# Kernel tuning notes

Hardware: AMD Instinct MI355X
Metric: run time of the kernel (lower is better)

Reference implementation:

```python
import jax, jax.numpy as jnp
import numpy as np

B, QL, KL, D, H = 2, 2048, 2048, 1024, 16
E = D // H  # head dim


def setup_inputs() -> dict:
    key = jax.random.key(0)
    ks = jax.random.split(key, 12)
    query_features = jax.random.normal(ks[0], (B, QL, D), dtype=jnp.float32)
    key_features = jax.random.normal(ks[1], (B, KL, D), dtype=jnp.float32)
    # causal additive mask [QL, KL]: -inf above the diagonal, 0 elsewhere
    dependency_mask = jnp.where(
        jnp.arange(KL)[None, :] > jnp.arange(QL)[:, None], -jnp.inf, 0.0
    ).astype(jnp.float32)
    # key padding: random valid lengths in [KL//2, KL]; True = padded position
    lengths = jax.random.randint(ks[2], (B,), KL // 2, KL + 1)
    key_padding_mask = jnp.arange(KL)[None, :] >= lengths[:, None]
    s = 0.02
    Wq = jax.random.normal(ks[3], (D, D), jnp.float32) * s
    bq = jax.random.normal(ks[4], (D,), jnp.float32) * s
    Wk = jax.random.normal(ks[5], (D, D), jnp.float32) * s
    bk = jax.random.normal(ks[6], (D,), jnp.float32) * s
    Wv = jax.random.normal(ks[7], (D, D), jnp.float32) * s
    bv = jax.random.normal(ks[8], (D,), jnp.float32) * s
    Wo = jax.random.normal(ks[9], (D, D), jnp.float32) * s
    bo = jax.random.normal(ks[10], (D,), jnp.float32) * s
    return dict(query_features=query_features, key_features=key_features,
                dependency_mask=dependency_mask, key_padding_mask=key_padding_mask,
                Wq=Wq, bq=bq, Wk=Wk, bk=bk, Wv=Wv, bv=bv, Wo=Wo, bo=bo)


def reference(query_features, key_features, dependency_mask, key_padding_mask,
              Wq, bq, Wk, bk, Wv, bv, Wo, bo):
    b, kl, d = key_features.shape
    ql = query_features.shape[1]
    q = query_features @ Wq.T + bq          # [B, QL, D]
    k = key_features @ Wk.T + bk            # [B, KL, D]
    v = key_features @ Wv.T + bv            # [B, KL, D]
    qh = q.reshape(b, ql, H, E)
    kh = k.reshape(b, kl, H, E)
    vh = v.reshape(b, kl, H, E)
    # NOTE: original scales by sqrt(d_model), not sqrt(head_dim)
    scores = jnp.einsum('bqhe,bkhe->bhqk', qh, kh) / jnp.sqrt(jnp.float32(d))
    scores = jnp.where(key_padding_mask[:, None, None, :], -jnp.inf, scores)
    scores = scores + dependency_mask  # broadcast [QL,KL] over [B,H,QL,KL]
    probs = jax.nn.softmax(scores, axis=-1)  # dropout is identity in eval mode
    agg = jnp.einsum('bhqk,bkhe->bqhe', probs, vh).reshape(b, ql, d)
    return agg @ Wo.T + bo
```

## Files before the change

### kernel.cpp

```cpp
#include <hip/hip_runtime.h>
#include <hip/hip_bf16.h>


typedef __bf16 bf16x8 __attribute__((ext_vector_type(8)));
typedef float f32x4 __attribute__((ext_vector_type(4)));
typedef unsigned int u32x4 __attribute__((ext_vector_type(4)));
typedef unsigned short u16;
typedef unsigned int u32;

#define GLOBAL_AS __attribute__((address_space(1)))
#define LDS_AS __attribute__((address_space(3)))

static __device__ __forceinline__ u16 f2bf(float f) {
    __hip_bfloat16 h = __float2bfloat16(f);
    return __builtin_bit_cast(u16, h);
}
static __device__ __forceinline__ u32 pack2bf(float a, float b) {
    return (u32)f2bf(a) | ((u32)f2bf(b) << 16);
}
static __device__ __forceinline__ float exp2_hw(float x) {
    return __builtin_amdgcn_exp2f(x);
}

__global__ void cvt_all(const float* __restrict__ xq_f, const float* __restrict__ xk_f,
                        const float* __restrict__ wq_f, const float* __restrict__ wk_f,
                        const float* __restrict__ wv_f, const float* __restrict__ wo_f,
                        u16* __restrict__ xq, u16* __restrict__ xk,
                        u16* __restrict__ wq, u16* __restrict__ wk,
                        u16* __restrict__ wv, u16* __restrict__ wo,
                        const int* __restrict__ kpm, int* __restrict__ lens) {
    int blk = blockIdx.x;
    if (blk >= 12288) {
        const int b = blk - 12288, tid = threadIdx.x;
        int cnt = 0;
        #pragma unroll
        for (int i = 0; i < 8; ++i) cnt += (kpm[b * 2048 + i * 256 + tid] == 0) ? 1 : 0;
        #pragma unroll
        for (int off = 32; off; off >>= 1) cnt += __shfl_down(cnt, off);
        __shared__ int wsum[4];
        if ((tid & 63) == 0) wsum[tid >> 6] = cnt;
        __syncthreads();
        if (tid == 0) lens[b] = wsum[0] + wsum[1] + wsum[2] + wsum[3];
        return;
    }
    const float* s; u16* d; int i;
    if (blk < 4096)      { s = xq_f; d = xq; i = blk * 256 + threadIdx.x; }
    else if (blk < 8192) { s = xk_f; d = xk; i = (blk - 4096) * 256 + threadIdx.x; }
    else {
        int wsel = (blk - 8192) >> 10;
        i = ((blk - 8192) & 1023) * 256 + threadIdx.x;
        if (wsel == 0)      { s = wq_f; d = wq; }
        else if (wsel == 1) { s = wk_f; d = wk; }
        else if (wsel == 2) { s = wv_f; d = wv; }
        else                { s = wo_f; d = wo; }
    }
    float4 v = reinterpret_cast<const float4*>(s)[i];
    ushort4 o;
    o.x = f2bf(v.x); o.y = f2bf(v.y); o.z = f2bf(v.z); o.w = f2bf(v.w);
    reinterpret_cast<ushort4*>(d)[i] = o;
}

template<int OUT_F32, int BM, int BN>
__device__ __forceinline__
void gemm_body(const u16* __restrict__ A, const u16* __restrict__ Bw,
               const float* __restrict__ bias, void* __restrict__ Cout,
               int N, int K, float scale, int bx, int by) {
    constexpr int MREP = BM / 32, NREP = BN / 32;
    constexpr int ACH = BM / 8, TCH = ACH + BN / 8;
    constexpr int CPW = TCH / 4;
    __shared__ __attribute__((aligned(16))) u16 aS[BM * 64];
    __shared__ __attribute__((aligned(16))) u16 bS[BN * 64];
    const int tid = threadIdx.x, wave = tid >> 6, lane = tid & 63;
    const int m0 = by * BM, n0 = bx * BN;
    const int wr = wave >> 1, wc = wave & 1;
    const int fr = lane & 15, fq = lane >> 4;
    const int swz_col = (((lane & 7) ^ (lane >> 3)) * 8);
    const int rsw = (fr & 7) << 3;

    f32x4 acc[MREP][NREP] = {};

    for (int k0 = 0; k0 < K; k0 += 64) {
        #pragma unroll
        for (int i = 0; i < CPW; ++i) {
            int chunk = wave * CPW + i;
            const u16* gsrc; u16* ldst;
            if (chunk < ACH) {
                int row = chunk * 8 + (lane >> 3);
                gsrc = A + (size_t)(m0 + row) * K + k0 + swz_col;
                ldst = aS + chunk * 512;
            } else {
                int row = (chunk - ACH) * 8 + (lane >> 3);
                gsrc = Bw + (size_t)(n0 + row) * K + k0 + swz_col;
                ldst = bS + (chunk - ACH) * 512;
            }
            __builtin_amdgcn_global_load_lds((GLOBAL_AS void*)gsrc,
                                             (LDS_AS void*)ldst, 16, 0, 0);
        }
        __syncthreads();
        bf16x8 af[MREP][2], bfr[NREP][2];
        #pragma unroll
        for (int m = 0; m < MREP; ++m)
            #pragma unroll
            for (int h = 0; h < 2; ++h)
                af[m][h] = *reinterpret_cast<const bf16x8*>(
                    &aS[(wr * (BM / 2) + m * 16 + fr) * 64 + ((h * 32 + fq * 8) ^ rsw)]);
        #pragma unroll
        for (int n = 0; n < NREP; ++n)
            #pragma unroll
            for (int h = 0; h < 2; ++h)
                bfr[n][h] = *reinterpret_cast<const bf16x8*>(
                    &bS[(wc * (BN / 2) + n * 16 + fr) * 64 + ((h * 32 + fq * 8) ^ rsw)]);
        __builtin_amdgcn_s_setprio(1);
        #pragma unroll
        for (int m = 0; m < MREP; ++m)
            #pragma unroll
            for (int n = 0; n < NREP; ++n) {
                acc[m][n] = __builtin_amdgcn_mfma_f32_16x16x32_bf16(af[m][0], bfr[n][0], acc[m][n], 0, 0, 0);
                acc[m][n] = __builtin_amdgcn_mfma_f32_16x16x32_bf16(af[m][1], bfr[n][1], acc[m][n], 0, 0, 0);
            }
        __builtin_amdgcn_s_setprio(0);
        __syncthreads();
    }

    #pragma unroll
    for (int n = 0; n < NREP; ++n) {
        int col = n0 + wc * (BN / 2) + n * 16 + fr;
        float bv = bias[col];
        #pragma unroll
        for (int m = 0; m < MREP; ++m) {
            #pragma unroll
            for (int j = 0; j < 4; ++j) {
                int row = m0 + wr * (BM / 2) + m * 16 + fq * 4 + j;
                float v = (acc[m][n][j] + bv) * scale;
                if (OUT_F32)
                    reinterpret_cast<float*>(Cout)[(size_t)row * N + col] = v;
                else
                    reinterpret_cast<u16*>(Cout)[(size_t)row * N + col] = f2bf(v);
            }
        }
    }
}

__global__ __launch_bounds__(256, 3)
void gemm_qkv(const u16* __restrict__ xq, const u16* __restrict__ xk,
              const u16* __restrict__ wq, const u16* __restrict__ wk,
              const u16* __restrict__ wv,
              const float* __restrict__ bq, const float* __restrict__ bk,
              const float* __restrict__ bv,
              u16* __restrict__ qb, u16* __restrict__ kb, u16* __restrict__ vb) {
    const int id = blockIdx.x;
    const int g = id & 7, s = id >> 3;
    const int z = s >> 5;
    const int xl = (s >> 3) & 3, byl = s & 7;
    const int bx = (g & 1) * 4 + xl;
    const int by = (g >> 1) * 8 + byl;
    const u16* A = (z == 0) ? xq : xk;
    const u16* W = (z == 0) ? wq : (z == 1) ? wk : wv;
    const float* bias = (z == 0) ? bq : (z == 1) ? bk : bv;
    u16* C = (z == 0) ? qb : (z == 1) ? kb : vb;
    const float scale = (z == 0) ? 0.0450842200f : 1.0f;
    gemm_body<0, 128, 128>(A, W, bias, C, 1024, 1024, scale, bx, by);
}

__global__ __launch_bounds__(256, 2)
void gemm_out(const u16* __restrict__ A, const u16* __restrict__ Bw,
              const float* __restrict__ bias, float* __restrict__ Cout) {
    const int id = blockIdx.x;
    const int g = id & 7, s = id >> 3;
    const int xl = s & 3, byl = s >> 2;
    const int bx = (g & 1) * 4 + xl;
    const int by = (g >> 1) * 16 + byl;
    gemm_body<1, 64, 128>(A, Bw, bias, Cout, 1024, 1024, 1.0f, bx, by);
}

__global__ __launch_bounds__(256, 4)
void attn_fwd(const u16* __restrict__ Qb, const u16* __restrict__ Kb,
              const u16* __restrict__ Vb, const int* __restrict__ lens,
              u16* __restrict__ Ob) {
    __shared__ __attribute__((aligned(16))) u16 Ks[2][64 * 64];
    __shared__ __attribute__((aligned(16))) u16 Vts[2][64 * 64];
    const int tid = threadIdx.x, wave = tid >> 6, lane = tid & 63;
    const int id = blockIdx.x;
    const int bh = (id & 7) * 4 + ((id >> 3) & 3);
    const int k5 = id >> 5;
    const int g = k5 >> 3, x8 = k5 & 7;
    const int qt = (g == 0) ? x8 : (g == 1) ? 31 - x8 : (g == 2) ? 16 + x8 : 15 - x8;
    const int b = bh >> 4, h = bh & 15;
    const int q0 = qt * 64;
    const int fr = lane & 15, fq = lane >> 4;
    const int qrow = q0 + wave * 16;
    const int len = lens[b];
    const int nt = min(qt + 1, (len + 63) >> 6);

    const size_t qoff = (size_t)(b * 2048 + qrow + fr) * 1024 + h * 64 + fq * 8;
    bf16x8 qa0 = *reinterpret_cast<const bf16x8*>(Qb + qoff);
    bf16x8 qa1 = *reinterpret_cast<const bf16x8*>(Qb + qoff + 32);

    bf16x8 ones;
    #pragma unroll
    for (int i = 0; i < 8; ++i) ones[i] = __builtin_bit_cast(__bf16, (u16)0x3F80);

    f32x4 o_acc[4] = {};
    f32x4 lacc = {};

    const int e8 = tid >> 5;
    const int c2 = tid & 31;
    const int kp = 2 * c2;
    const int vhalf = kp >> 5, r5 = kp & 31;
    const int fqv = r5 >> 3, nv = (r5 >> 2) & 1, jv = r5 & 3;
    const int k_src = vhalf * 32 + nv * 16 + fqv * 4 + jv;
    const int kswz_col = (((lane & 7) ^ (lane >> 3)) * 8);

    auto issue_K = [&](int kt, int buf) {
        #pragma unroll
        for (int i = 0; i < 2; ++i) {
            int chunk = wave * 2 + i;
            int krow = chunk * 8 + (lane >> 3);
            const u16* gk = Kb + (size_t)(b * 2048 + kt * 64 + krow) * 1024 + h * 64 + kswz_col;
            __builtin_amdgcn_global_load_lds((GLOBAL_AS void*)gk,
                                             (LDS_AS void*)(&Ks[buf][chunk * 512]), 16, 0, 0);
        }
    };
    auto load_V = [&](int kt, ushort4* r) {
        const u16* b1 = Vb + (size_t)(b * 2048 + kt * 64 + k_src) * 1024 + h * 64 + e8 * 8;
        r[0] = reinterpret_cast<const ushort4*>(b1)[0];
        r[1] = reinterpret_cast<const ushort4*>(b1 + 4)[0];
        r[2] = reinterpret_cast<const ushort4*>(b1 + 1024)[0];
        r[3] = reinterpret_cast<const ushort4*>(b1 + 1024 + 4)[0];
    };
    auto write_V = [&](const ushort4* r, int buf) {
        u32* vbase = reinterpret_cast<u32*>(&Vts[buf][0]);
        const u16* lo16 = reinterpret_cast<const u16*>(&r[0]);
        const u16* hi16 = reinterpret_cast<const u16*>(&r[2]);
        #pragma unroll
        for (int i = 0; i < 8; ++i) {
            u32 w = (u32)lo16[i] | ((u32)hi16[i] << 16);
            vbase[(e8 * 8 + i) * 32 + (c2 ^ (i << 2))] = w;
        }
    };

    {
        ushort4 vr[4];
        issue_K(0, 0);
        load_V(0, vr);
        write_V(vr, 0);
    }
    __syncthreads();

    for (int kt = 0; kt < nt; ++kt) {
        const int k0 = kt * 64;
        const int cur = kt & 1, nxt = cur ^ 1;
        const bool has_next = (kt + 1 < nt);

        ushort4 vr[4];
        if (has_next) {
            issue_K(kt + 1, nxt);
            load_V(kt + 1, vr);
        }

        f32x4 s[4] = {};
        __builtin_amdgcn_s_setprio(1);
        #pragma unroll
        for (int n = 0; n < 4; ++n) {
            int kr = n * 16 + fr;
            int sw = (fr & 7) << 3;
            bf16x8 kb0 = *reinterpret_cast<const bf16x8*>(&Ks[cur][kr * 64 + ((fq * 8) ^ sw)]);
            bf16x8 kb1 = *reinterpret_cast<const bf16x8*>(&Ks[cur][kr * 64 + ((32 + fq * 8) ^ sw)]);
            s[n] = __builtin_amdgcn_mfma_f32_16x16x32_bf16(kb0, qa0, s[n], 0, 0, 0);
            s[n] = __builtin_amdgcn_mfma_f32_16x16x32_bf16(kb1, qa1, s[n], 0, 0, 0);
        }
        __builtin_amdgcn_s_setprio(0);

        const bool fullt = (k0 + 63 <= qrow) && (k0 + 64 <= len);
        if (!fullt) {
            const int qg = qrow + fr;
            #pragma unroll
            for (int n = 0; n < 4; ++n)
                #pragma unroll
                for (int j = 0; j < 4; ++j) {
                    int kg = k0 + n * 16 + fq * 4 + j;
                    s[n][j] = (kg <= qg && kg < len) ? s[n][j] : -1e30f;
                }
        }
        #pragma unroll
        for (int n = 0; n < 4; ++n)
            #pragma unroll
            for (int j = 0; j < 4; ++j)
                s[n][j] = exp2_hw(s[n][j]);

        u32x4 w0, w1;
        w0[0] = pack2bf(s[0][0], s[0][1]); w0[1] = pack2bf(s[0][2], s[0][3]);
        w0[2] = pack2bf(s[1][0], s[1][1]); w0[3] = pack2bf(s[1][2], s[1][3]);
        w1[0] = pack2bf(s[2][0], s[2][1]); w1[1] = pack2bf(s[2][2], s[2][3]);
        w1[2] = pack2bf(s[3][0], s[3][1]); w1[3] = pack2bf(s[3][2], s[3][3]);
        bf16x8 pa0 = __builtin_bit_cast(bf16x8, w0);
        bf16x8 pa1 = __builtin_bit_cast(bf16x8, w1);

        if (has_next) write_V(vr, nxt);

        __builtin_amdgcn_s_setprio(1);
        lacc = __builtin_amdgcn_mfma_f32_16x16x32_bf16(pa0, ones, lacc, 0, 0, 0);
        #pragma unroll
        for (int n = 0; n < 4; ++n) {
            int vr2 = n * 16 + fr;
            bf16x8 vb2 = *reinterpret_cast<const bf16x8*>(
                &Vts[cur][vr2 * 64 + ((fq * 8) ^ ((fr & 7) << 3))]);
            o_acc[n] = __builtin_amdgcn_mfma_f32_16x16x32_bf16(pa0, vb2, o_acc[n], 0, 0, 0);
        }
        lacc = __builtin_amdgcn_mfma_f32_16x16x32_bf16(pa1, ones, lacc, 0, 0, 0);
        #pragma unroll
        for (int n = 0; n < 4; ++n) {
            int vr2 = n * 16 + fr;
            bf16x8 vb2 = *reinterpret_cast<const bf16x8*>(
                &Vts[cur][vr2 * 64 + ((32 + fq * 8) ^ ((fr & 7) << 3))]);
            o_acc[n] = __builtin_amdgcn_mfma_f32_16x16x32_bf16(pa1, vb2, o_acc[n], 0, 0, 0);
        }
        __builtin_amdgcn_s_setprio(0);

        __syncthreads();
    }

    #pragma unroll
    for (int j = 0; j < 4; ++j) {
        float inv = 1.f / lacc[j];
        int row = qrow + fq * 4 + j;
        #pragma unroll
        for (int n = 0; n < 4; ++n) {
            int col = h * 64 + n * 16 + fr;
            Ob[(size_t)(b * 2048 + row) * 1024 + col] = f2bf(o_acc[n][j] * inv);
        }
    }
}

extern "C" void kernel_launch(void* const* d_in, const int* in_sizes, int n_in,
                              void* d_out, int out_size, void* d_ws, size_t ws_size,
                              hipStream_t stream) {
    const float* xq_f = (const float*)d_in[0];
    const float* xk_f = (const float*)d_in[1];
    const int* kpm = (const int*)d_in[3];
    const float* Wq = (const float*)d_in[4];
    const float* bq = (const float*)d_in[5];
    const float* Wk = (const float*)d_in[6];
    const float* bk = (const float*)d_in[7];
    const float* Wv = (const float*)d_in[8];
    const float* bv = (const float*)d_in[9];
    const float* Wo = (const float*)d_in[10];
    const float* bo = (const float*)d_in[11];

    u16* ws = (u16*)d_ws;
    u16* xq = ws;
    u16* xk = xq + 4194304;
    u16* wq = xk + 4194304;
    u16* wk = wq + 1048576;
    u16* wv = wk + 1048576;
    u16* wo = wv + 1048576;
    u16* qb = wo + 1048576;
    u16* kb2 = qb + 4194304;
    u16* vb2 = kb2 + 4194304;
    u16* ag = vb2 + 4194304;
    int* lens = (int*)(ag + 4194304);

    cvt_all<<<12290, 256, 0, stream>>>(xq_f, xk_f, Wq, Wk, Wv, Wo,
                                       xq, xk, wq, wk, wv, wo, kpm, lens);

    gemm_qkv<<<768, 256, 0, stream>>>(xq, xk, wq, wk, wv,
                                      bq, bk, bv, qb, kb2, vb2);

    attn_fwd<<<1024, 256, 0, stream>>>(qb, kb2, vb2, lens, ag);

    gemm_out<<<512, 256, 0, stream>>>(ag, wo, bo, (float*)d_out);
}
```

Before: 100.6 us.

## Split attention tile across waves by key halves with LDS reduction

Each wave now handles 32 query rows against one 32-key half of each 64-key tile, instead of 16 query rows against all 64 keys. Every K and V fragment read from LDS is then reused for two query groups, which halves per-wave LDS fragment traffic. The price is a final cross-wave reduction of the partial O and row sums through LDS, with extra barriers, and more accumulator registers per wave.

```diff
diff --git a/kernel.cpp b/kernel.cpp
--- a/kernel.cpp
+++ b/kernel.cpp
@@ -186,22 +186,27 @@
     const int g = k5 >> 3, x8 = k5 & 7;
     const int qt = (g == 0) ? x8 : (g == 1) ? 31 - x8 : (g == 2) ? 16 + x8 : 15 - x8;
     const int b = bh >> 4, h = bh & 15;
-    const int q0 = qt * 64;
     const int fr = lane & 15, fq = lane >> 4;
-    const int qrow = q0 + wave * 16;
+    const int t = wave >> 1;
+    const int u = wave & 1;
+    const int qbase = qt * 64 + u * 32;
     const int len = lens[b];
     const int nt = min(qt + 1, (len + 63) >> 6);
 
-    const size_t qoff = (size_t)(b * 2048 + qrow + fr) * 1024 + h * 64 + fq * 8;
-    bf16x8 qa0 = *reinterpret_cast<const bf16x8*>(Qb + qoff);
-    bf16x8 qa1 = *reinterpret_cast<const bf16x8*>(Qb + qoff + 32);
+    bf16x8 qa[2][2];
+    #pragma unroll
+    for (int gq = 0; gq < 2; ++gq) {
+        const size_t qoff = (size_t)(b * 2048 + qbase + gq * 16 + fr) * 1024 + h * 64 + fq * 8;
+        qa[gq][0] = *reinterpret_cast<const bf16x8*>(Qb + qoff);
+        qa[gq][1] = *reinterpret_cast<const bf16x8*>(Qb + qoff + 32);
+    }
 
     bf16x8 ones;
     #pragma unroll
     for (int i = 0; i < 8; ++i) ones[i] = __builtin_bit_cast(__bf16, (u16)0x3F80);
 
-    f32x4 o_acc[4] = {};
-    f32x4 lacc = {};
+    f32x4 o_acc[2][4] = {};
+    f32x4 lacc[2] = {};
 
     const int e8 = tid >> 5;
     const int c2 = tid & 31;
@@ -249,6 +254,7 @@
 
     for (int kt = 0; kt < nt; ++kt) {
         const int k0 = kt * 64;
+        const int kbase = k0 + t * 32;
         const int cur = kt & 1, nxt = cur ^ 1;
         const bool has_next = (kt + 1 < nt);
 
@@ -258,77 +264,107 @@
             load_V(kt + 1, vr);
         }
 
-        f32x4 s[4] = {};
+        f32x4 s[2][2] = {};
         __builtin_amdgcn_s_setprio(1);
         #pragma unroll
-        for (int n = 0; n < 4; ++n) {
-            int kr = n * 16 + fr;
+        for (int kq2 = 0; kq2 < 2; ++kq2) {
+            int kr = t * 32 + kq2 * 16 + fr;
             int sw = (fr & 7) << 3;
             bf16x8 kb0 = *reinterpret_cast<const bf16x8*>(&Ks[cur][kr * 64 + ((fq * 8) ^ sw)]);
             bf16x8 kb1 = *reinterpret_cast<const bf16x8*>(&Ks[cur][kr * 64 + ((32 + fq * 8) ^ sw)]);
-            s[n] = __builtin_amdgcn_mfma_f32_16x16x32_bf16(kb0, qa0, s[n], 0, 0, 0);
-            s[n] = __builtin_amdgcn_mfma_f32_16x16x32_bf16(kb1, qa1, s[n], 0, 0, 0);
+            #pragma unroll
+            for (int gq = 0; gq < 2; ++gq) {
+                s[kq2][gq] = __builtin_amdgcn_mfma_f32_16x16x32_bf16(kb0, qa[gq][0], s[kq2][gq], 0, 0, 0);
+                s[kq2][gq] = __builtin_amdgcn_mfma_f32_16x16x32_bf16(kb1, qa[gq][1], s[kq2][gq], 0, 0, 0);
+            }
         }
         __builtin_amdgcn_s_setprio(0);
 
-        const bool fullt = (k0 + 63 <= qrow) && (k0 + 64 <= len);
+        const bool fullt = (kbase + 31 <= qbase) && (kbase + 32 <= len);
         if (!fullt) {
-            const int qg = qrow + fr;
-            #pragma unroll
-            for (int n = 0; n < 4; ++n)
+            #pragma unroll
+            for (int kq2 = 0; kq2 < 2; ++kq2)
                 #pragma unroll
-                for (int j = 0; j < 4; ++j) {
-                    int kg = k0 + n * 16 + fq * 4 + j;
-                    s[n][j] = (kg <= qg && kg < len) ? s[n][j] : -1e30f;
+                for (int gq = 0; gq < 2; ++gq) {
+                    int qg = qbase + gq * 16 + fr;
+                    #pragma unroll
+                    for (int j = 0; j < 4; ++j) {
+                        int kg = kbase + kq2 * 16 + fq * 4 + j;
+                        s[kq2][gq][j] = (kg <= qg && kg < len) ? s[kq2][gq][j] : -1e30f;
+                    }
                 }
         }
         #pragma unroll
-        for (int n = 0; n < 4; ++n)
-            #pragma unroll
-            for (int j = 0; j < 4; ++j)
-                s[n][j] = exp2_hw(s[n][j]);
-
-        u32x4 w0, w1;
-        w0[0] = pack2bf(s[0][0], s[0][1]); w0[1] = pack2bf(s[0][2], s[0][3]);
-        w0[2] = pack2bf(s[1][0], s[1][1]); w0[3] = pack2bf(s[1][2], s[1][3]);
-        w1[0] = pack2bf(s[2][0], s[2][1]); w1[1] = pack2bf(s[2][2], s[2][3]);
-        w1[2] = pack2bf(s[3][0], s[3][1]); w1[3] = pack2bf(s[3][2], s[3][3]);
-        bf16x8 pa0 = __builtin_bit_cast(bf16x8, w0);
-        bf16x8 pa1 = __builtin_bit_cast(bf16x8, w1);
+        for (int kq2 = 0; kq2 < 2; ++kq2)
+            #pragma unroll
+            for (int gq = 0; gq < 2; ++gq)
+                #pragma unroll
+                for (int j = 0; j < 4; ++j)
+                    s[kq2][gq][j] = exp2_hw(s[kq2][gq][j]);
+
+        bf16x8 pa[2];
+        #pragma unroll
+        for (int gq = 0; gq < 2; ++gq) {
+            u32x4 w;
+            w[0] = pack2bf(s[0][gq][0], s[0][gq][1]);
+            w[1] = pack2bf(s[0][gq][2], s[0][gq][3]);
+            w[2] = pack2bf(s[1][gq][0], s[1][gq][1]);
+            w[3] = pack2bf(s[1][gq][2], s[1][gq][3]);
+            pa[gq] = __builtin_bit_cast(bf16x8, w);
+        }
 
         if (has_next) write_V(vr, nxt);
 
         __builtin_amdgcn_s_setprio(1);
-        lacc = __builtin_amdgcn_mfma_f32_16x16x32_bf16(pa0, ones, lacc, 0, 0, 0);
+        bf16x8 vbr[4];
         #pragma unroll
         for (int n = 0; n < 4; ++n) {
             int vr2 = n * 16 + fr;
-            bf16x8 vb2 = *reinterpret_cast<const bf16x8*>(
-                &Vts[cur][vr2 * 64 + ((fq * 8) ^ ((fr & 7) << 3))]);
-            o_acc[n] = __builtin_amdgcn_mfma_f32_16x16x32_bf16(pa0, vb2, o_acc[n], 0, 0, 0);
-        }
-        lacc = __builtin_amdgcn_mfma_f32_16x16x32_bf16(pa1, ones, lacc, 0, 0, 0);
-        #pragma unroll
-        for (int n = 0; n < 4; ++n) {
-            int vr2 = n * 16 + fr;
-            bf16x8 vb2 = *reinterpret_cast<const bf16x8*>(
-                &Vts[cur][vr2 * 64 + ((32 + fq * 8) ^ ((fr & 7) << 3))]);
-            o_acc[n] = __builtin_amdgcn_mfma_f32_16x16x32_bf16(pa1, vb2, o_acc[n], 0, 0, 0);
+            vbr[n] = *reinterpret_cast<const bf16x8*>(
+                &Vts[cur][vr2 * 64 + ((t * 32 + fq * 8) ^ ((fr & 7) << 3))]);
+        }
+        #pragma unroll
+        for (int gq = 0; gq < 2; ++gq) {
+            lacc[gq] = __builtin_amdgcn_mfma_f32_16x16x32_bf16(pa[gq], ones, lacc[gq], 0, 0, 0);
+            #pragma unroll
+            for (int n = 0; n < 4; ++n)
+                o_acc[gq][n] = __builtin_amdgcn_mfma_f32_16x16x32_bf16(pa[gq], vbr[n], o_acc[gq][n], 0, 0, 0);
         }
         __builtin_amdgcn_s_setprio(0);
 
         __syncthreads();
     }
 
-    #pragma unroll
-    for (int j = 0; j < 4; ++j) {
-        float inv = 1.f / lacc[j];
-        int row = qrow + fq * 4 + j;
-        #pragma unroll
-        for (int n = 0; n < 4; ++n) {
-            int col = h * 64 + n * 16 + fr;
-            Ob[(size_t)(b * 2048 + row) * 1024 + col] = f2bf(o_acc[n][j] * inv);
-        }
+    __syncthreads();
+    float* ocomb = reinterpret_cast<float*>(&Ks[0][0]);
+    float* lcomb = reinterpret_cast<float*>(&Vts[0][0]);
+    if (t == 1) {
+        #pragma unroll
+        for (int gq = 0; gq < 2; ++gq)
+            #pragma unroll
+            for (int j = 0; j < 4; ++j) {
+                int ql = u * 32 + gq * 16 + fq * 4 + j;
+                #pragma unroll
+                for (int n = 0; n < 4; ++n)
+                    ocomb[ql * 64 + n * 16 + fr] = o_acc[gq][n][j];
+                if (fr == 0) lcomb[ql] = lacc[gq][j];
+            }
+    }
+    __syncthreads();
+    if (t == 0) {
+        #pragma unroll
+        for (int gq = 0; gq < 2; ++gq)
+            #pragma unroll
+            for (int j = 0; j < 4; ++j) {
+                int ql = u * 32 + gq * 16 + fq * 4 + j;
+                float inv = 1.f / (lacc[gq][j] + lcomb[ql]);
+                int row = qt * 64 + ql;
+                #pragma unroll
+                for (int n = 0; n < 4; ++n) {
+                    float osum = o_acc[gq][n][j] + ocomb[ql * 64 + n * 16 + fr];
+                    Ob[(size_t)(b * 2048 + row) * 1024 + h * 64 + n * 16 + fr] = f2bf(osum * inv);
+                }
+            }
     }
 }
 
```

After: 99.31 us. About the same (-1.3%).
